# Kernel tuning notes

Measured on AMD Instinct MI355X. Metric: run time of the kernel, lower is better.

## Reference

```python
import jax, jax.numpy as jnp
import numpy as np

K = 9          # kernel_size (odd)
STRIDE = 1
EPS = 1e-12


def _unfold(x, k, stride, pad):
    # x: (bs, ch, H, W) -> (bs, ch, k, k, out_h, out_w); mimics F.unfold + view.
    bs, ch, H, W = x.shape
    out_h = (H + 2 * pad - k) // stride + 1
    out_w = (W + 2 * pad - k) // stride + 1
    xp = jnp.pad(x, ((0, 0), (0, 0), (pad, pad), (pad, pad)))
    rows = []
    for dy in range(k):  # fixed small loop over kernel taps
        row = [xp[:, :, dy:dy + out_h * stride:stride, dx:dx + out_w * stride:stride]
               for dx in range(k)]
        rows.append(jnp.stack(row, axis=2))
    return jnp.stack(rows, axis=2)


def setup_inputs() -> dict:
    key = jax.random.key(0)
    k1, k2 = jax.random.split(key)
    inp = jax.random.normal(k1, (2, 3, 384, 384), dtype=jnp.float32)
    sigmas = jax.random.uniform(k2, (2, 2, 384, 384), dtype=jnp.float32)
    return {"input": inp, "sigmas": sigmas}


def reference(input, sigmas):
    k, s = K, STRIDE
    pad = k // 2
    dt = input.dtype
    # inverse sigmas on strided grid
    sig_s = 1.0 / (jnp.abs(sigmas[:, 0:1, ::s, ::s]) + EPS)  # (bs,1,oh,ow)
    sig_r = 1.0 / (jnp.abs(sigmas[:, 1:2, ::s, ::s]) + EPS)
    # spatial Gaussian kernel, per-pixel sigma
    r = jnp.arange(-(k // 2), k // 2 + 1, dtype=dt)
    _1d = -0.5 * r * r
    _2d = (_1d[:, None] + _1d[None, :]).reshape(1, 1, k, k, 1, 1)
    g = jnp.exp(_2d * (sig_s * sig_s)[:, :, None, None, :, :])  # (bs,1,k,k,oh,ow)
    g = g / g.sum(axis=(2, 3), keepdims=True)
    # range (guide) Gaussian from local diff^2 summed over channels
    cols = _unfold(input, k, s, pad)                          # (bs,ch,k,k,oh,ow)
    center = cols[:, :, k // 2:k // 2 + 1, k // 2:k // 2 + 1]
    diff_sq = jnp.sum((cols - center) ** 2, axis=1, keepdims=True)
    guide = jnp.exp(-0.5 * diff_sq * (sig_r * sig_r)[:, :, None, None, :, :])
    # combine, normalize (guard empty windows), apply
    kmg = g * guide
    norm = kmg.sum(axis=(2, 3), keepdims=True)
    kmg = kmg / (norm + (norm == 0).astype(dt))
    out = jnp.sum(cols * kmg, axis=(2, 3))                    # (bs,ch,oh,ow)
    return out
```

## Files before the change

kernel.cpp:

```cpp
#include <hip/hip_runtime.h>
#include <hip/hip_bf16.h>

typedef float f32x2 __attribute__((ext_vector_type(2)));

#define IMG_H 384
#define IMG_W 384
#define KSZ 9
#define KR 4
#define TW 16
#define TH 8
#define NP (TW/2)
#define HW (TW + 2*KR)
#define HH (TH + 2*KR)
#define PST 37
#define PLANE (IMG_H * IMG_W)

static __device__ __forceinline__ f32x2 mk2(float a, float b) { f32x2 r; r.x = a; r.y = b; return r; }

__global__ __launch_bounds__(192) void abf_kernel(
    const float* __restrict__ input,
    const float* __restrict__ sigmas,
    float* __restrict__ out)
{
    __shared__ float s_in[3 * HH * PST];
    __shared__ f32x2 s_comb[2][NP * TH][4];

    const int b      = blockIdx.z;
    const int tile_x = blockIdx.x * TW;
    const int tile_y = blockIdx.y * TH;
    const int tx = threadIdx.x;
    const int ty = threadIdx.y;
    const int tz = threadIdx.z;
    const int tid = (tz * TH + ty) * NP + tx;

    {
        const int sy = tid / HW;
        const int sx = tid - sy * HW;
        const int gx = tile_x + sx - KR;
        const bool okx = (gx >= 0) & (gx < IMG_W);
        const float* inb = input + (size_t)b * 3 * PLANE;
        #pragma unroll
        for (int c = 0; c < 3; ++c) {
            #pragma unroll
            for (int k = 0; k < 2; ++k) {
                const int y  = sy + 8 * k;
                const int gy = tile_y + y - KR;
                float v = 0.f;
                if (okx & (gy >= 0) & (gy < IMG_H))
                    v = inb[c * PLANE + (gy << 8) + (gy << 7) + gx];
                s_in[(c * HH + y) * PST + sx] = v;
            }
        }
    }
    __syncthreads();

    const int lx = 2 * tx;
    const int ox = tile_x + lx;
    const int oy = tile_y + ty;

    const float* sgb = sigmas + (size_t)b * 2 * PLANE;
    const int sidx = (oy << 8) + (oy << 7) + ox;
    const float sA0 = sgb[sidx],          sB0 = sgb[sidx + 1];
    const float sA1 = sgb[PLANE + sidx],  sB1 = sgb[PLANE + sidx + 1];
    const float isA = __builtin_amdgcn_rcpf(fabsf(sA0) + 1e-12f);
    const float isB = __builtin_amdgcn_rcpf(fabsf(sB0) + 1e-12f);
    const float irA = __builtin_amdgcn_rcpf(fabsf(sA1) + 1e-12f);
    const float irB = __builtin_amdgcn_rcpf(fabsf(sB1) + 1e-12f);
    const f32x2 A = mk2(-0.72134752f * isA * isA, -0.72134752f * isB * isB);
    const f32x2 B = mk2(-0.72134752f * irA * irA, -0.72134752f * irB * irB);

    const int cb = (ty + KR) * PST + lx + KR;
    const f32x2 cen0 = mk2(s_in[0 * HH * PST + cb], s_in[0 * HH * PST + cb + 1]);
    const f32x2 cen1 = mk2(s_in[1 * HH * PST + cb], s_in[1 * HH * PST + cb + 1]);
    const f32x2 cen2 = mk2(s_in[2 * HH * PST + cb], s_in[2 * HH * PST + cb + 1]);

    f32x2 wsum = mk2(0.f, 0.f), a0 = wsum, a1 = wsum, a2 = wsum;

    #pragma unroll 1
    for (int r = 0; r < 3; ++r) {
        const int dy = tz * 3 + r;
        const float ry2 = (float)((dy - KR) * (dy - KR));
        const f32x2 syA = ry2 * A;
        const int r0 = (0 * HH + ty + dy) * PST + lx;
        const int r1 = (1 * HH + ty + dy) * PST + lx;
        const int r2 = (2 * HH + ty + dy) * PST + lx;

        float w0[10], w1[10], w2[10];
        #pragma unroll
        for (int j = 0; j < 10; ++j) {
            w0[j] = s_in[r0 + j];
            w1[j] = s_in[r1 + j];
            w2[j] = s_in[r2 + j];
        }

        #pragma unroll
        for (int dx = 0; dx < KSZ; ++dx) {
            const float rx2 = (float)((dx - KR) * (dx - KR));
            const f32x2 v0 = mk2(w0[dx], w0[dx + 1]);
            const f32x2 v1 = mk2(w1[dx], w1[dx + 1]);
            const f32x2 v2 = mk2(w2[dx], w2[dx + 1]);
            const f32x2 d0 = v0 - cen0;
            const f32x2 d1 = v1 - cen1;
            const f32x2 d2 = v2 - cen2;
            const f32x2 dsq = d0 * d0 + d1 * d1 + d2 * d2;
            const f32x2 arg = dsq * B + (rx2 * A + syA);
            const f32x2 w = mk2(__builtin_amdgcn_exp2f(arg.x),
                                __builtin_amdgcn_exp2f(arg.y));
            wsum += w;
            a0 += w * v0;
            a1 += w * v1;
            a2 += w * v2;
        }
    }

    const int pid = ty * NP + tx;
    if (tz > 0) {
        s_comb[tz - 1][pid][0] = wsum;
        s_comb[tz - 1][pid][1] = a0;
        s_comb[tz - 1][pid][2] = a1;
        s_comb[tz - 1][pid][3] = a2;
    }
    __syncthreads();

    if (tz == 0) {
        #pragma unroll
        for (int t = 0; t < 2; ++t) {
            wsum += s_comb[t][pid][0];
            a0   += s_comb[t][pid][1];
            a1   += s_comb[t][pid][2];
            a2   += s_comb[t][pid][3];
        }
        const f32x2 inv = mk2(__builtin_amdgcn_rcpf(wsum.x),
                              __builtin_amdgcn_rcpf(wsum.y));
        float* outb = out + (size_t)b * 3 * PLANE;
        const int oidx = (oy << 8) + (oy << 7) + ox;
        const f32x2 o0 = a0 * inv, o1 = a1 * inv, o2 = a2 * inv;
        *reinterpret_cast<float2*>(&outb[oidx])             = make_float2(o0.x, o0.y);
        *reinterpret_cast<float2*>(&outb[PLANE + oidx])     = make_float2(o1.x, o1.y);
        *reinterpret_cast<float2*>(&outb[2 * PLANE + oidx]) = make_float2(o2.x, o2.y);
    }
}

extern "C" void kernel_launch(void* const* d_in, const int* in_sizes, int n_in,
                              void* d_out, int out_size, void* d_ws, size_t ws_size,
                              hipStream_t stream) {
    const float* input  = (const float*)d_in[0];
    const float* sigmas = (const float*)d_in[1];
    float* out = (float*)d_out;

    dim3 block(NP, TH, 3);
    dim3 grid(IMG_W / TW, IMG_H / TH, 2);
    abf_kernel<<<grid, block, 0, stream>>>(input, sigmas, out);
}
```

Before: 16.44 us.

## Pair vertically adjacent pixels per thread with even/odd row-interleaved shared layout

Each thread now computes two vertically adjacent output pixels instead of two horizontal ones. The input tile is stored in shared memory as float2 pairs of rows, split into even- and odd-offset copies, so each tap becomes a single 64-bit LDS load of both pixels' values. This is meant to remove the scalar shared loads and register shuffling needed to build horizontal pairs. In exchange it duplicates the halo in shared memory and turns the output and sigma accesses into scalar, row-strided global accesses.

```diff
diff --git a/kernel.cpp b/kernel.cpp
--- a/kernel.cpp
+++ b/kernel.cpp
@@ -3,17 +3,16 @@
 
 typedef float f32x2 __attribute__((ext_vector_type(2)));
 
-#define IMG_H 384
-#define IMG_W 384
-#define KSZ 9
+#define IMG 384
 #define KR 4
 #define TW 16
 #define TH 8
-#define NP (TW/2)
-#define HW (TW + 2*KR)
-#define HH (TH + 2*KR)
-#define PST 37
-#define PLANE (IMG_H * IMG_W)
+#define HW 24
+#define HH 16
+#define PRS 25
+#define NE 8
+#define NO 7
+#define PLANE (IMG*IMG)
 
 static __device__ __forceinline__ f32x2 mk2(float a, float b) { f32x2 r; r.x = a; r.y = b; return r; }
 
@@ -22,8 +21,9 @@
     const float* __restrict__ sigmas,
     float* __restrict__ out)
 {
-    __shared__ float s_in[3 * HH * PST];
-    __shared__ f32x2 s_comb[2][NP * TH][4];
+    __shared__ f32x2 sE[3 * NE * PRS];
+    __shared__ f32x2 sO[3 * NO * PRS];
+    __shared__ f32x2 s_comb[2][TW * (TH/2)][4];
 
     const int b      = blockIdx.z;
     const int tile_x = blockIdx.x * TW;
@@ -31,74 +31,80 @@
     const int tx = threadIdx.x;
     const int ty = threadIdx.y;
     const int tz = threadIdx.z;
-    const int tid = (tz * TH + ty) * NP + tx;
+    const int tid = tz * 64 + ty * TW + tx;
 
     {
         const int sy = tid / HW;
         const int sx = tid - sy * HW;
         const int gx = tile_x + sx - KR;
-        const bool okx = (gx >= 0) & (gx < IMG_W);
+        const bool okx = (gx >= 0) & (gx < IMG);
         const float* inb = input + (size_t)b * 3 * PLANE;
+        float* fE = (float*)sE;
+        float* fO = (float*)sO;
         #pragma unroll
         for (int c = 0; c < 3; ++c) {
             #pragma unroll
             for (int k = 0; k < 2; ++k) {
-                const int y  = sy + 8 * k;
-                const int gy = tile_y + y - KR;
+                const int hy = sy + 8 * k;
+                const int gy = tile_y + hy - KR;
                 float v = 0.f;
-                if (okx & (gy >= 0) & (gy < IMG_H))
+                if (okx & (gy >= 0) & (gy < IMG))
                     v = inb[c * PLANE + (gy << 8) + (gy << 7) + gx];
-                s_in[(c * HH + y) * PST + sx] = v;
+                fE[((c * NE + (hy >> 1)) * PRS + sx) * 2 + (hy & 1)] = v;
+                if (hy >= 1 && hy <= 14)
+                    fO[((c * NO + ((hy - 1) >> 1)) * PRS + sx) * 2 + ((hy - 1) & 1)] = v;
             }
         }
     }
     __syncthreads();
 
-    const int lx = 2 * tx;
-    const int ox = tile_x + lx;
-    const int oy = tile_y + ty;
+    const int ox  = tile_x + tx;
+    const int oyA = tile_y + 2 * ty;
+    const int siA = (oyA << 8) + (oyA << 7) + ox;
 
     const float* sgb = sigmas + (size_t)b * 2 * PLANE;
-    const int sidx = (oy << 8) + (oy << 7) + ox;
-    const float sA0 = sgb[sidx],          sB0 = sgb[sidx + 1];
-    const float sA1 = sgb[PLANE + sidx],  sB1 = sgb[PLANE + sidx + 1];
-    const float isA = __builtin_amdgcn_rcpf(fabsf(sA0) + 1e-12f);
-    const float isB = __builtin_amdgcn_rcpf(fabsf(sB0) + 1e-12f);
-    const float irA = __builtin_amdgcn_rcpf(fabsf(sA1) + 1e-12f);
-    const float irB = __builtin_amdgcn_rcpf(fabsf(sB1) + 1e-12f);
+    const float ssA = sgb[siA],         ssB = sgb[siA + IMG];
+    const float srA = sgb[PLANE + siA], srB = sgb[PLANE + siA + IMG];
+    const float isA = __builtin_amdgcn_rcpf(fabsf(ssA) + 1e-12f);
+    const float isB = __builtin_amdgcn_rcpf(fabsf(ssB) + 1e-12f);
+    const float irA = __builtin_amdgcn_rcpf(fabsf(srA) + 1e-12f);
+    const float irB = __builtin_amdgcn_rcpf(fabsf(srB) + 1e-12f);
     const f32x2 A = mk2(-0.72134752f * isA * isA, -0.72134752f * isB * isB);
     const f32x2 B = mk2(-0.72134752f * irA * irA, -0.72134752f * irB * irB);
 
-    const int cb = (ty + KR) * PST + lx + KR;
-    const f32x2 cen0 = mk2(s_in[0 * HH * PST + cb], s_in[0 * HH * PST + cb + 1]);
-    const f32x2 cen1 = mk2(s_in[1 * HH * PST + cb], s_in[1 * HH * PST + cb + 1]);
-    const f32x2 cen2 = mk2(s_in[2 * HH * PST + cb], s_in[2 * HH * PST + cb + 1]);
+    const f32x2 cen0 = sE[(0 * NE + ty + 2) * PRS + tx + 4];
+    const f32x2 cen1 = sE[(1 * NE + ty + 2) * PRS + tx + 4];
+    const f32x2 cen2 = sE[(2 * NE + ty + 2) * PRS + tx + 4];
 
     f32x2 wsum = mk2(0.f, 0.f), a0 = wsum, a1 = wsum, a2 = wsum;
 
     #pragma unroll 1
     for (int r = 0; r < 3; ++r) {
         const int dy = tz * 3 + r;
-        const float ry2 = (float)((dy - KR) * (dy - KR));
-        const f32x2 syA = ry2 * A;
-        const int r0 = (0 * HH + ty + dy) * PST + lx;
-        const int r1 = (1 * HH + ty + dy) * PST + lx;
-        const int r2 = (2 * HH + ty + dy) * PST + lx;
+        const float ry = (float)(dy - KR);
+        const f32x2 syA = (ry * ry) * A;
 
-        float w0[10], w1[10], w2[10];
-        #pragma unroll
-        for (int j = 0; j < 10; ++j) {
-            w0[j] = s_in[r0 + j];
-            w1[j] = s_in[r1 + j];
-            w2[j] = s_in[r2 + j];
+        const f32x2 *p0, *p1, *p2;
+        if (dy & 1) {
+            const int pr = ty + ((dy - 1) >> 1);
+            p0 = &sO[(0 * NO + pr) * PRS + tx];
+            p1 = &sO[(1 * NO + pr) * PRS + tx];
+            p2 = &sO[(2 * NO + pr) * PRS + tx];
+        } else {
+            const int pr = ty + (dy >> 1);
+            p0 = &sE[(0 * NE + pr) * PRS + tx];
+            p1 = &sE[(1 * NE + pr) * PRS + tx];
+            p2 = &sE[(2 * NE + pr) * PRS + tx];
         }
 
+        f32x2 w0[9], w1[9], w2[9];
         #pragma unroll
-        for (int dx = 0; dx < KSZ; ++dx) {
+        for (int j = 0; j < 9; ++j) { w0[j] = p0[j]; w1[j] = p1[j]; w2[j] = p2[j]; }
+
+        #pragma unroll
+        for (int dx = 0; dx < 9; ++dx) {
             const float rx2 = (float)((dx - KR) * (dx - KR));
-            const f32x2 v0 = mk2(w0[dx], w0[dx + 1]);
-            const f32x2 v1 = mk2(w1[dx], w1[dx + 1]);
-            const f32x2 v2 = mk2(w2[dx], w2[dx + 1]);
+            const f32x2 v0 = w0[dx], v1 = w1[dx], v2 = w2[dx];
             const f32x2 d0 = v0 - cen0;
             const f32x2 d1 = v1 - cen1;
             const f32x2 d2 = v2 - cen2;
@@ -113,7 +119,7 @@
         }
     }
 
-    const int pid = ty * NP + tx;
+    const int pid = ty * TW + tx;
     if (tz > 0) {
         s_comb[tz - 1][pid][0] = wsum;
         s_comb[tz - 1][pid][1] = a0;
@@ -133,11 +139,10 @@
         const f32x2 inv = mk2(__builtin_amdgcn_rcpf(wsum.x),
                               __builtin_amdgcn_rcpf(wsum.y));
         float* outb = out + (size_t)b * 3 * PLANE;
-        const int oidx = (oy << 8) + (oy << 7) + ox;
         const f32x2 o0 = a0 * inv, o1 = a1 * inv, o2 = a2 * inv;
-        *reinterpret_cast<float2*>(&outb[oidx])             = make_float2(o0.x, o0.y);
-        *reinterpret_cast<float2*>(&outb[PLANE + oidx])     = make_float2(o1.x, o1.y);
-        *reinterpret_cast<float2*>(&outb[2 * PLANE + oidx]) = make_float2(o2.x, o2.y);
+        outb[siA]                 = o0.x;  outb[siA + IMG]             = o0.y;
+        outb[PLANE + siA]         = o1.x;  outb[PLANE + siA + IMG]     = o1.y;
+        outb[2 * PLANE + siA]     = o2.x;  outb[2 * PLANE + siA + IMG] = o2.y;
     }
 }
 
@@ -148,7 +153,7 @@
     const float* sigmas = (const float*)d_in[1];
     float* out = (float*)d_out;
 
-    dim3 block(NP, TH, 3);
-    dim3 grid(IMG_W / TW, IMG_H / TH, 2);
+    dim3 block(TW, TH / 2, 3);
+    dim3 grid(IMG / TW, IMG / TH, 2);
     abf_kernel<<<grid, block, 0, stream>>>(input, sigmas, out);
 }
```

Result: faster. 15.63 us, median of 2 (-4.9%).
